# Kernel optimization log

Hardware: AMD Instinct MI355X
Metric: run time of the kernel (lower is better)

Reference implementation:

```python
import jax, jax.numpy as jnp
import numpy as np

NUM_NODES = 100000
HIDDEN = 128
HEADS = 4
NUM_EDGES = 1600000
NUM_PAIRS = 100000


def _leaky_relu(x, slope=0.2):
    return jnp.where(x >= 0, x, slope * x)


def _gat_layer(x, W, a_src, a_dst, src, dst):
    # x: [N, D]; W: [D, H*Dh]; a_src/a_dst: [H, Dh]
    N = x.shape[0]
    H, Dh = a_src.shape
    h = (x @ W).reshape(N, H, Dh)
    hs = h[src]                                   # [E, H, Dh] gather
    e = _leaky_relu((hs * a_src).sum(-1) + (h[dst] * a_dst).sum(-1))  # [E, H]
    # torch scatter_reduce amax over a zeros buffer => max clamped at 0
    m = jnp.maximum(jax.ops.segment_max(e, dst, num_segments=N), 0.0)  # [N, H]
    a = jnp.exp(e - m[dst])
    s = jax.ops.segment_sum(a, dst, num_segments=N)
    a = a / (s[dst] + 1e-10)
    out = jax.ops.segment_sum(hs * a[..., None], dst, num_segments=N)  # [N, H, Dh]
    return out.reshape(N, H * Dh)


def setup_inputs() -> dict:
    key = jax.random.key(0)
    ks = jax.random.split(key, 16)
    N, D, H = NUM_NODES, HIDDEN, HEADS
    Dh = D // H
    sW = float(np.sqrt(6.0 / (D + D)))
    sa = float(np.sqrt(6.0 / (H + Dh)))
    inp = {
        'embed': jax.random.uniform(ks[0], (N, D), jnp.float32, -sW, sW),
        'W1': jax.random.uniform(ks[1], (D, D), jnp.float32, -sW, sW),
        'a_src1': jax.random.uniform(ks[2], (H, Dh), jnp.float32, -sa, sa),
        'a_dst1': jax.random.uniform(ks[3], (H, Dh), jnp.float32, -sa, sa),
        'W2': jax.random.uniform(ks[4], (D, D), jnp.float32, -sW, sW),
        'a_src2': jax.random.uniform(ks[5], (H, Dh), jnp.float32, -sa, sa),
        'a_dst2': jax.random.uniform(ks[6], (H, Dh), jnp.float32, -sa, sa),
        'lp_w1': jax.random.uniform(ks[7], (2 * D, D), jnp.float32, -sW, sW),
        'lp_b1': jnp.zeros((D,), jnp.float32),
        'lp_w2': jax.random.uniform(ks[8], (D, 1), jnp.float32, -sW, sW),
        'lp_b2': jnp.zeros((1,), jnp.float32),
        'edge_index': jax.random.randint(ks[9], (2, NUM_EDGES), 0, N, jnp.int64 if jax.config.jax_enable_x64 else jnp.int32),
        'link_src': jax.random.randint(ks[10], (NUM_PAIRS,), 0, N),
        'link_dst': jax.random.randint(ks[11], (NUM_PAIRS,), 0, N),
    }
    return inp


def reference(embed, W1, a_src1, a_dst1, W2, a_src2, a_dst2,
              lp_w1, lp_b1, lp_w2, lp_b2, edge_index, link_src, link_dst):
    src, dst = edge_index[0], edge_index[1]
    x = embed
    x = jax.nn.elu(_gat_layer(x, W1, a_src1, a_dst1, src, dst)) + x
    x = jax.nn.elu(_gat_layer(x, W2, a_src2, a_dst2, src, dst)) + x
    z = x
    hcat = jnp.concatenate([z[link_src], z[link_dst]], axis=-1)  # [P, 2D]
    hid = jax.nn.relu(hcat @ lp_w1 + lp_b1)
    logits = (hid @ lp_w2 + lp_b2).squeeze(-1)  # [P]
    return logits
```

## Files before the change

### kernel.cpp

```cpp
#include <hip/hip_runtime.h>

typedef unsigned short u16;
typedef unsigned int u32;
typedef __attribute__((ext_vector_type(8))) short short8;
typedef __attribute__((ext_vector_type(4))) float float4v;

#define N_NODES 100000
#define N_EDGES 1600000
#define N_PAIRS 100000
#define NBUCKP 256
#define NB_USED 196
#define BUCK_CAP 8704
#define BIN_GRID 391

__device__ __forceinline__ float bf2f(u32 lo16) {
    union { u32 u; float f; } v;
    v.u = lo16 << 16;
    return v.f;
}
__device__ __forceinline__ u16 f2bf(float f) {
    union { float f; u32 u; } v;
    v.f = f;
    u32 r = v.u + 0x7fffu + ((v.u >> 16) & 1u);
    return (u16)(r >> 16);
}

#define FMIX_LO(A, Q, W) asm("v_fma_mix_f32 %0, %1, %2, %0 op_sel:[0,0,0] op_sel_hi:[1,1,0]" : "+v"(A) : "v"(Q), "v"(W))
#define FMIX_HI(A, Q, W) asm("v_fma_mix_f32 %0, %1, %2, %0 op_sel:[1,0,0] op_sel_hi:[1,1,0]" : "+v"(A) : "v"(Q), "v"(W))

__global__ __launch_bounds__(256) void k_prepB4(const float* __restrict__ W1, const float* __restrict__ W2,
                                                const float* __restrict__ WA, const float* __restrict__ WB,
                                                u16* __restrict__ B1, u16* __restrict__ B2,
                                                u16* __restrict__ BA, u16* __restrict__ BB,
                                                int* __restrict__ bucket_cur) {
    if (blockIdx.x == 32) {
        bucket_cur[threadIdx.x] = threadIdx.x * BUCK_CAP;
        return;
    }
    int w = blockIdx.x >> 3;
    const float* W = (w == 0) ? W1 : (w == 1) ? W2 : (w == 2) ? WA : WB;
    u16* Bf = (w == 0) ? B1 : (w == 1) ? B2 : (w == 2) ? BA : BB;
    int t = (blockIdx.x & 7) * 256 + threadIdx.x;
    int kk = t >> 9, tn = (t >> 6) & 7, quad = (t >> 4) & 3, l15 = t & 15;
#pragma unroll
    for (int j = 0; j < 8; j++) {
        int k = kk * 32 + quad * 8 + j;
        int n = tn * 16 + l15;
        Bf[(size_t)t * 8 + j] = f2bf(W[k * 128 + n]);
    }
}

__global__ __launch_bounds__(256) void k_bin(const int* __restrict__ esrc, const int* __restrict__ edst,
                                             int* bucket_cur, int2* __restrict__ binned) {
    __shared__ int cnt[NBUCKP];
    __shared__ int base[NBUCKP];
    int t = threadIdx.x;
    cnt[t] = 0;
    __syncthreads();
    int s[16], d[16], r[16];
    int e0 = blockIdx.x * 4096;
#pragma unroll
    for (int k = 0; k < 16; k++) {
        int e = e0 + k * 256 + t;
        if (e < N_EDGES) {
            s[k] = esrc[e];
            d[k] = edst[e];
            r[k] = atomicAdd(&cnt[d[k] >> 9], 1);
        } else {
            d[k] = -1;
        }
    }
    __syncthreads();
    base[t] = cnt[t] ? atomicAdd(&bucket_cur[t], cnt[t]) : 0;
    __syncthreads();
#pragma unroll
    for (int k = 0; k < 16; k++) {
        if (d[k] >= 0) {
            int bk = d[k] >> 9;
            int pos = base[bk] + r[k];
            if (pos < (bk + 1) * BUCK_CAP)
                binned[pos] = make_int2(s[k], d[k]);
        }
    }
}

__global__ __launch_bounds__(512) void k_sort(const int2* __restrict__ binned,
                                              const int* __restrict__ bucket_cur,
                                              int* __restrict__ row_ptr,
                                              int* __restrict__ col_src) {
    __shared__ int cnt[512];
    __shared__ int sm[512];
    int b = blockIdx.x, t = threadIdx.x;

    int partial = 0;
    if (t < b) partial = bucket_cur[t] - t * BUCK_CAP;
    sm[t] = partial;
    __syncthreads();
    for (int o = 256; o >= 1; o >>= 1) {
        if (t < o) sm[t] += sm[t + o];
        __syncthreads();
    }
    int base = sm[0];
    int n_e = bucket_cur[b] - b * BUCK_CAP;
    if (n_e > BUCK_CAP) n_e = BUCK_CAP;
    __syncthreads();

    cnt[t] = 0;
    __syncthreads();
    const int2* ebase = binned + (size_t)b * BUCK_CAP;
    for (int i = t; i < n_e; i += 512)
        atomicAdd(&cnt[ebase[i].y & 511], 1);
    __syncthreads();
    int v = cnt[t];
    sm[t] = v;
    __syncthreads();
    for (int o = 1; o < 512; o <<= 1) {
        int x = (t >= o) ? sm[t - o] : 0;
        __syncthreads();
        sm[t] += x;
        __syncthreads();
    }
    int excl = base + sm[t] - v;
    int node = b * 512 + t;
    if (node <= N_NODES) row_ptr[node] = excl;
    cnt[t] = excl;
    __syncthreads();
    for (int i = t; i < n_e; i += 512) {
        int2 sd = ebase[i];
        int p = atomicAdd(&cnt[sd.y & 511], 1);
        col_src[p] = sd.x;
    }
}

template<bool AF32, bool DUAL, bool QUANT>
__global__ __launch_bounds__(256) void k_gemm(const void* __restrict__ Ap,
                                              const u16* __restrict__ Bf,
                                              const u16* __restrict__ Bf2,
                                              u16* __restrict__ C,
                                              u16* __restrict__ C2,
                                              char* __restrict__ hq,
                                              float* __restrict__ alsc,
                                              const float* __restrict__ a_src,
                                              const float* __restrict__ a_dst,
                                              float* __restrict__ al_d, int M) {
    int wave = threadIdx.x >> 6, lane = threadIdx.x & 63;
    int quad = lane >> 4, l15 = lane & 15;
    int row0 = blockIdx.x * 64 + wave * 16;
    int m = row0 + l15;
    int mload = (m < M) ? m : (M - 1);

    short8 a[4];
    if (AF32) {
        const float* A = (const float*)Ap;
#pragma unroll
        for (int kk = 0; kk < 4; kk++) {
            const float* p = A + (size_t)mload * 128 + kk * 32 + quad * 8;
            float4 f0 = *(const float4*)p;
            float4 f1 = *(const float4*)(p + 4);
            short8 av;
            av[0] = (short)f2bf(f0.x); av[1] = (short)f2bf(f0.y);
            av[2] = (short)f2bf(f0.z); av[3] = (short)f2bf(f0.w);
            av[4] = (short)f2bf(f1.x); av[5] = (short)f2bf(f1.y);
            av[6] = (short)f2bf(f1.z); av[7] = (short)f2bf(f1.w);
            a[kk] = av;
        }
    } else {
        const u16* A = (const u16*)Ap;
#pragma unroll
        for (int kk = 0; kk < 4; kk++)
            a[kk] = *(const short8*)(A + (size_t)mload * 128 + kk * 32 + quad * 8);
    }

    float4v acc[8], acc2[8];
#pragma unroll
    for (int tn = 0; tn < 8; tn++) {
        acc[tn] = (float4v){0.f, 0.f, 0.f, 0.f};
        if (DUAL) acc2[tn] = (float4v){0.f, 0.f, 0.f, 0.f};
    }

#pragma unroll
    for (int kk = 0; kk < 4; kk++) {
#pragma unroll
        for (int tn = 0; tn < 8; tn++) {
            short8 b = *(const short8*)(Bf + ((size_t)((kk * 8 + tn) * 64 + lane)) * 8);
            acc[tn] = __builtin_amdgcn_mfma_f32_16x16x32_bf16(a[kk], b, acc[tn], 0, 0, 0);
            if (DUAL) {
                short8 b2 = *(const short8*)(Bf2 + ((size_t)((kk * 8 + tn) * 64 + lane)) * 8);
                acc2[tn] = __builtin_amdgcn_mfma_f32_16x16x32_bf16(a[kk], b2, acc2[tn], 0, 0, 0);
            }
        }
    }

    float as0[4], as1[4], ad0[4], ad1[4];
    if (QUANT) {
#pragma unroll
        for (int hd = 0; hd < 4; hd++) {
            as0[hd] = a_src[hd * 32 + l15];
            as1[hd] = a_src[hd * 32 + 16 + l15];
            ad0[hd] = a_dst[hd * 32 + l15];
            ad1[hd] = a_dst[hd * 32 + 16 + l15];
        }
    }

#pragma unroll
    for (int rg = 0; rg < 4; rg++) {
        int gr = row0 + quad * 4 + rg;
        bool ok = (gr < M);
        if (!QUANT) {
            if (ok) {
#pragma unroll
                for (int tn = 0; tn < 8; tn++) {
                    C[(size_t)gr * 128 + tn * 16 + l15] = f2bf(acc[tn][rg]);
                    if (DUAL) C2[(size_t)gr * 128 + tn * 16 + l15] = f2bf(acc2[tn][rg]);
                }
            }
        } else {
            float amax = 0.f;
#pragma unroll
            for (int tn = 0; tn < 8; tn++) amax = fmaxf(amax, fabsf(acc[tn][rg]));
#pragma unroll
            for (int mm = 1; mm < 16; mm <<= 1) amax = fmaxf(amax, __shfl_xor(amax, mm, 64));
            float inv_s = (amax > 0.f) ? 127.f / amax : 0.f;
            if (ok) {
#pragma unroll
                for (int tn = 0; tn < 8; tn++) {
                    int q = (int)rintf(acc[tn][rg] * inv_s);
                    hq[(size_t)gr * 128 + tn * 16 + l15] = (char)(q + 128);
                }
            }
            float ps[4], pd[4];
#pragma unroll
            for (int hd = 0; hd < 4; hd++) {
                float c0 = acc[2 * hd][rg];
                float c1 = acc[2 * hd + 1][rg];
                ps[hd] = c0 * as0[hd] + c1 * as1[hd];
                pd[hd] = c0 * ad0[hd] + c1 * ad1[hd];
            }
#pragma unroll
            for (int mm = 1; mm < 16; mm <<= 1) {
#pragma unroll
                for (int hd = 0; hd < 4; hd++) {
                    ps[hd] += __shfl_xor(ps[hd], mm, 64);
                    pd[hd] += __shfl_xor(pd[hd], mm, 64);
                }
            }
            if (ok && l15 < 4) {
                float vs = (l15 == 0) ? ps[0] : (l15 == 1) ? ps[1] : (l15 == 2) ? ps[2] : ps[3];
                float vd = (l15 == 0) ? pd[0] : (l15 == 1) ? pd[1] : (l15 == 2) ? pd[2] : pd[3];
                alsc[(size_t)gr * 8 + l15 * 2]     = vs;
                alsc[(size_t)gr * 8 + l15 * 2 + 1] = amax * (1.f / 127.f);
                al_d[gr * 4 + l15] = vd;
            }
        }
    }
}

template<bool XF32>
__global__ __launch_bounds__(256) void k_agg(const int* __restrict__ row_ptr, const int* __restrict__ col_src,
                      const float* __restrict__ alsc, const float* __restrict__ al_d,
                      const char* __restrict__ hq,
                      const void* __restrict__ xin, u16* __restrict__ xout) {
    int node = blockIdx.x * 4 + (threadIdx.x >> 6);
    int lane = threadIdx.x & 63;
    int l15 = lane & 15;
    int grp = lane >> 4;
    int bh  = l15 >> 2;
    int ae  = lane >> 2;
    int ah  = lane & 3;
    int beg = row_ptr[node], end = row_ptr[node + 1];
    int deg = end - beg;
    int degm1 = (deg > 0) ? deg - 1 : 0;
    float adst = al_d[node * 4 + ah];
    u32 loff = (u32)(l15 * 8);

    float sw = 0.f, swl = 0.f;
    u32 h_one = 0x3C00u;
    float acc[8];
#pragma unroll
    for (int k = 0; k < 8; k++) acc[k] = 0.f;

    int nch = (deg + 15) >> 4;
    for (int cb = 0; cb < nch; cb++) {
        int c = cb * 16;
        int idx = c + l15;
        idx = (idx <= degm1) ? idx : degm1;
        int sv = col_src[beg + idx];

        int sA = __shfl(sv, ae, 64);
        float2 av = *(const float2*)(alsc + ((size_t)sA << 3) + (ah << 1));
        float ev = av.x + adst;
        ev = fmaxf(ev, 0.2f * ev);
        float w = __expf(ev);
        w = ((c + ae) < deg) ? w : 0.f;
        sw += w;
        float wsc = w * av.y;

#pragma unroll
        for (int i = 0; i < 4; i++) {
            int slot = 4 * i + grp;
            int s = __shfl(sv, slot, 64);
            float wl = __shfl(wsc, slot * 4 + bh, 64);
            u32 wlh;
            asm("v_cvt_f16_f32 %0, %1" : "=v"(wlh) : "v"(wl));
            FMIX_LO(swl, h_one, wlh);
            u32 off = ((u32)s << 7) + loff;
            uint2 hv = *(const uint2*)(hq + off);
            u32 p01 = __builtin_amdgcn_perm(0x64646464u, hv.x, 0x04010400u);
            u32 p23 = __builtin_amdgcn_perm(0x64646464u, hv.x, 0x04030402u);
            u32 p45 = __builtin_amdgcn_perm(0x64646464u, hv.y, 0x04010400u);
            u32 p67 = __builtin_amdgcn_perm(0x64646464u, hv.y, 0x04030402u);
            FMIX_LO(acc[0], p01, wlh); FMIX_HI(acc[1], p01, wlh);
            FMIX_LO(acc[2], p23, wlh); FMIX_HI(acc[3], p23, wlh);
            FMIX_LO(acc[4], p45, wlh); FMIX_HI(acc[5], p45, wlh);
            FMIX_LO(acc[6], p67, wlh); FMIX_HI(acc[7], p67, wlh);
        }
    }

#pragma unroll
    for (int k = 0; k < 8; k++) acc[k] = fmaf(swl, -1152.f, acc[k]);

#pragma unroll
    for (int mm = 4; mm < 64; mm <<= 1) sw += __shfl_xor(sw, mm, 64);
    float inv = 1.f / (__shfl(sw, bh, 64) + 1e-10f);

#pragma unroll
    for (int k = 0; k < 8; k++) {
        acc[k] += __shfl_xor(acc[k], 16, 64);
        acc[k] += __shfl_xor(acc[k], 32, 64);
    }

    if (grp == 0) {
        float r[8];
        if (XF32) {
            const float* x = (const float*)xin;
            float4 x0 = *(const float4*)&x[(size_t)node * 128 + l15 * 8];
            float4 x1 = *(const float4*)&x[(size_t)node * 128 + l15 * 8 + 4];
            r[0] = x0.x; r[1] = x0.y; r[2] = x0.z; r[3] = x0.w;
            r[4] = x1.x; r[5] = x1.y; r[6] = x1.z; r[7] = x1.w;
        } else {
            const u16* x = (const u16*)xin;
            short8 xv = *(const short8*)&x[(size_t)node * 128 + l15 * 8];
#pragma unroll
            for (int k = 0; k < 8; k++) r[k] = bf2f((u16)xv[k]);
        }
        u32 ow[4];
#pragma unroll
        for (int k = 0; k < 4; k++) {
            float a0 = acc[2 * k] * inv;
            float a1 = acc[2 * k + 1] * inv;
            a0 = (a0 > 0.f) ? a0 : (__expf(a0) - 1.f);
            a1 = (a1 > 0.f) ? a1 : (__expf(a1) - 1.f);
            ow[k] = (u32)f2bf(a0 + r[2 * k]) | ((u32)f2bf(a1 + r[2 * k + 1]) << 16);
        }
        *(uint4*)&xout[(size_t)node * 128 + l15 * 8] = make_uint4(ow[0], ow[1], ow[2], ow[3]);
    }
}

__global__ void k_pair(const int* __restrict__ psrc, const int* __restrict__ pdst,
                       const u16* __restrict__ u, const u16* __restrict__ v,
                       const float* __restrict__ b1, const float* __restrict__ w2,
                       const float* __restrict__ b2, float* __restrict__ out) {
    int p = blockIdx.x * 4 + (threadIdx.x >> 6);
    int lane = threadIdx.x & 63;
    int s = psrc[p], d = pdst[p];
    float h0 = bf2f(u[(size_t)s * 128 + lane * 2])     + bf2f(v[(size_t)d * 128 + lane * 2])     + b1[lane * 2];
    float h1 = bf2f(u[(size_t)s * 128 + lane * 2 + 1]) + bf2f(v[(size_t)d * 128 + lane * 2 + 1]) + b1[lane * 2 + 1];
    h0 = (h0 > 0.f) ? h0 : 0.f;
    h1 = (h1 > 0.f) ? h1 : 0.f;
    float acc = h0 * w2[lane * 2] + h1 * w2[lane * 2 + 1];
#pragma unroll
    for (int m = 1; m < 64; m <<= 1) acc += __shfl_xor(acc, m, 64);
    if (lane == 0) out[p] = acc + b2[0];
}

extern "C" void kernel_launch(void* const* d_in, const int* in_sizes, int n_in,
                              void* d_out, int out_size, void* d_ws, size_t ws_size,
                              hipStream_t stream) {
    const float* embed  = (const float*)d_in[0];
    const float* W1     = (const float*)d_in[1];
    const float* a_src1 = (const float*)d_in[2];
    const float* a_dst1 = (const float*)d_in[3];
    const float* W2     = (const float*)d_in[4];
    const float* a_src2 = (const float*)d_in[5];
    const float* a_dst2 = (const float*)d_in[6];
    const float* lp_w1  = (const float*)d_in[7];
    const float* lp_b1  = (const float*)d_in[8];
    const float* lp_w2  = (const float*)d_in[9];
    const float* lp_b2  = (const float*)d_in[10];
    const int*   edge   = (const int*)d_in[11];
    const int*   lsrc   = (const int*)d_in[12];
    const int*   ldst   = (const int*)d_in[13];
    float* out = (float*)d_out;

    char* ws = (char*)d_ws;
    size_t off = 0;
    auto alloc = [&](size_t bytes) -> char* {
        char* p = ws + off;
        off += (bytes + 255) & ~(size_t)255;
        return p;
    };
    int*  row_ptr    = (int*)alloc((N_NODES + 1) * 4);
    int*  bucket_cur = (int*)alloc(NBUCKP * 4);
    int2* binned     = (int2*)alloc((size_t)NBUCKP * BUCK_CAP * 8);
    int*  col_src    = (int*)alloc((size_t)N_EDGES * 4);
    char* hq         = (char*)alloc((size_t)N_NODES * 128);
    float* alsc      = (float*)alloc((size_t)N_NODES * 8 * 4);
    float* al_d      = (float*)alloc((size_t)N_NODES * 4 * 4);
    u16*  x1         = (u16*)alloc((size_t)N_NODES * 128 * 2);
    u16*  z          = (u16*)alloc((size_t)N_NODES * 128 * 2);
    u16*  uu         = (u16*)alloc((size_t)N_NODES * 128 * 2);
    u16*  vv         = (u16*)alloc((size_t)N_NODES * 128 * 2);
    u16*  Bf1        = (u16*)alloc(128 * 128 * 2);
    u16*  Bf2        = (u16*)alloc(128 * 128 * 2);
    u16*  BfA        = (u16*)alloc(128 * 128 * 2);
    u16*  BfB        = (u16*)alloc(128 * 128 * 2);

    const int* esrc = edge;
    const int* edst = edge + N_EDGES;
    const int GB = (N_NODES + 63) / 64;

    k_prepB4<<<33, 256, 0, stream>>>(W1, W2, lp_w1, lp_w1 + 128 * 128, Bf1, Bf2, BfA, BfB, bucket_cur);

    k_bin <<<BIN_GRID, 256, 0, stream>>>(esrc, edst, bucket_cur, binned);
    k_sort<<<NB_USED, 512, 0, stream>>>(binned, bucket_cur, row_ptr, col_src);

    k_gemm<true, false, true><<<GB, 256, 0, stream>>>(embed, Bf1, nullptr, nullptr, nullptr,
                                                      hq, alsc, a_src1, a_dst1, al_d, N_NODES);
    k_agg<true><<<N_NODES / 4, 256, 0, stream>>>(row_ptr, col_src, alsc, al_d, hq, embed, x1);
    k_gemm<false, false, true><<<GB, 256, 0, stream>>>(x1, Bf2, nullptr, nullptr, nullptr,
                                                       hq, alsc, a_src2, a_dst2, al_d, N_NODES);
    k_agg<false><<<N_NODES / 4, 256, 0, stream>>>(row_ptr, col_src, alsc, al_d, hq, x1, z);
    k_gemm<false, true, false><<<GB, 256, 0, stream>>>(z, BfA, BfB, uu, vv,
                                                       nullptr, nullptr, nullptr, nullptr, nullptr, N_NODES);
    k_pair<<<N_PAIRS / 4, 256, 0, stream>>>(lsrc, ldst, uu, vv, lp_b1, lp_w2, lp_b2, out);
}
```

Baseline: 356.2 us.

## Unroll GAT aggregation for first 32 edges with all gathers issued upfront

Replaces the chunked 16-edge loop in the aggregation kernel with a fixed 32-edge prologue. All col_src, attention-score and feature-row gathers are issued before any use, which raises memory-level parallelism for typical degree-16 nodes. Edges past 32 go through a scalar per-edge tail loop, and zero-degree nodes exit early after writing the residual. The residual input load is hoisted to the start so its latency overlaps with the gathers. In exchange, nodes with fewer than 32 edges now do redundant clamped loads, and register pressure rises from the 8 outstanding feature loads.

```diff
diff --git a/kernel.cpp b/kernel.cpp
--- a/kernel.cpp
+++ b/kernel.cpp
@@ -269,46 +269,112 @@
     int ah  = lane & 3;
     int beg = row_ptr[node], end = row_ptr[node + 1];
     int deg = end - beg;
-    int degm1 = (deg > 0) ? deg - 1 : 0;
+    u32 loff = (u32)(l15 * 8);
+
+    float r[8];
+    if (XF32) {
+        const float* x = (const float*)xin;
+        float4 x0 = *(const float4*)&x[(size_t)node * 128 + l15 * 8];
+        float4 x1 = *(const float4*)&x[(size_t)node * 128 + l15 * 8 + 4];
+        r[0] = x0.x; r[1] = x0.y; r[2] = x0.z; r[3] = x0.w;
+        r[4] = x1.x; r[5] = x1.y; r[6] = x1.z; r[7] = x1.w;
+    } else {
+        const u16* x = (const u16*)xin;
+        short8 xv = *(const short8*)&x[(size_t)node * 128 + l15 * 8];
+#pragma unroll
+        for (int k = 0; k < 8; k++) r[k] = bf2f((u16)xv[k]);
+    }
+
+    if (deg == 0) {
+        if (grp == 0) {
+            u32 ow[4];
+#pragma unroll
+            for (int k = 0; k < 4; k++)
+                ow[k] = (u32)f2bf(r[2 * k]) | ((u32)f2bf(r[2 * k + 1]) << 16);
+            *(uint4*)&xout[(size_t)node * 128 + l15 * 8] = make_uint4(ow[0], ow[1], ow[2], ow[3]);
+        }
+        return;
+    }
+    int degm1 = deg - 1;
     float adst = al_d[node * 4 + ah];
-    u32 loff = (u32)(l15 * 8);
-
-    float sw = 0.f, swl = 0.f;
+
+    int slotA0 = (ae <= degm1) ? ae : degm1;
+    int slotA1 = (ae + 16 <= degm1) ? ae + 16 : degm1;
+    int sA0 = col_src[beg + slotA0];
+    int sA1 = col_src[beg + slotA1];
+    int sB[8];
+#pragma unroll
+    for (int i = 0; i < 8; i++) {
+        int slot = i * 4 + grp;
+        slot = (slot <= degm1) ? slot : degm1;
+        sB[i] = col_src[beg + slot];
+    }
+
+    float2 avA0 = *(const float2*)(alsc + ((size_t)sA0 << 3) + (ah << 1));
+    float2 avA1 = *(const float2*)(alsc + ((size_t)sA1 << 3) + (ah << 1));
+    uint2 hv[8];
+#pragma unroll
+    for (int i = 0; i < 8; i++)
+        hv[i] = *(const uint2*)(hq + (((u32)sB[i]) << 7) + loff);
+
+    float ev0 = avA0.x + adst;
+    ev0 = fmaxf(ev0, 0.2f * ev0);
+    float w0 = __expf(ev0);
+    w0 = (ae < deg) ? w0 : 0.f;
+    float ev1 = avA1.x + adst;
+    ev1 = fmaxf(ev1, 0.2f * ev1);
+    float w1 = __expf(ev1);
+    w1 = (ae + 16 < deg) ? w1 : 0.f;
+    float sw = w0 + w1;
+    float wsc0 = w0 * avA0.y;
+    float wsc1 = w1 * avA1.y;
+
+#pragma unroll
+    for (int mm = 4; mm < 64; mm <<= 1) sw += __shfl_xor(sw, mm, 64);
+
+    float swl = 0.f;
     u32 h_one = 0x3C00u;
     float acc[8];
 #pragma unroll
     for (int k = 0; k < 8; k++) acc[k] = 0.f;
 
-    int nch = (deg + 15) >> 4;
-    for (int cb = 0; cb < nch; cb++) {
-        int c = cb * 16;
-        int idx = c + l15;
-        idx = (idx <= degm1) ? idx : degm1;
-        int sv = col_src[beg + idx];
-
-        int sA = __shfl(sv, ae, 64);
-        float2 av = *(const float2*)(alsc + ((size_t)sA << 3) + (ah << 1));
-        float ev = av.x + adst;
-        ev = fmaxf(ev, 0.2f * ev);
-        float w = __expf(ev);
-        w = ((c + ae) < deg) ? w : 0.f;
-        sw += w;
-        float wsc = w * av.y;
-
-#pragma unroll
-        for (int i = 0; i < 4; i++) {
-            int slot = 4 * i + grp;
-            int s = __shfl(sv, slot, 64);
-            float wl = __shfl(wsc, slot * 4 + bh, 64);
+#pragma unroll
+    for (int i = 0; i < 8; i++) {
+        int slot = i * 4 + grp;
+        float wl = (i < 4) ? __shfl(wsc0, slot * 4 + bh, 64)
+                           : __shfl(wsc1, (slot - 16) * 4 + bh, 64);
+        u32 wlh;
+        asm("v_cvt_f16_f32 %0, %1" : "=v"(wlh) : "v"(wl));
+        FMIX_LO(swl, h_one, wlh);
+        u32 p01 = __builtin_amdgcn_perm(0x64646464u, hv[i].x, 0x04010400u);
+        u32 p23 = __builtin_amdgcn_perm(0x64646464u, hv[i].x, 0x04030402u);
+        u32 p45 = __builtin_amdgcn_perm(0x64646464u, hv[i].y, 0x04010400u);
+        u32 p67 = __builtin_amdgcn_perm(0x64646464u, hv[i].y, 0x04030402u);
+        FMIX_LO(acc[0], p01, wlh); FMIX_HI(acc[1], p01, wlh);
+        FMIX_LO(acc[2], p23, wlh); FMIX_HI(acc[3], p23, wlh);
+        FMIX_LO(acc[4], p45, wlh); FMIX_HI(acc[5], p45, wlh);
+        FMIX_LO(acc[6], p67, wlh); FMIX_HI(acc[7], p67, wlh);
+    }
+
+    float swt = 0.f;
+    if (deg > 32) {
+        float adstB = al_d[node * 4 + bh];
+        for (int i = 32; i < deg; i++) {
+            int s = __builtin_amdgcn_readfirstlane(col_src[beg + i]);
+            float2 av = *(const float2*)(alsc + ((size_t)s << 3) + (bh << 1));
+            float ev = av.x + adstB;
+            ev = fmaxf(ev, 0.2f * ev);
+            float w = __expf(ev);
+            swt += w;
+            float wl = (grp == 0) ? w * av.y : 0.f;
             u32 wlh;
             asm("v_cvt_f16_f32 %0, %1" : "=v"(wlh) : "v"(wl));
             FMIX_LO(swl, h_one, wlh);
-            u32 off = ((u32)s << 7) + loff;
-            uint2 hv = *(const uint2*)(hq + off);
-            u32 p01 = __builtin_amdgcn_perm(0x64646464u, hv.x, 0x04010400u);
-            u32 p23 = __builtin_amdgcn_perm(0x64646464u, hv.x, 0x04030402u);
-            u32 p45 = __builtin_amdgcn_perm(0x64646464u, hv.y, 0x04010400u);
-            u32 p67 = __builtin_amdgcn_perm(0x64646464u, hv.y, 0x04030402u);
+            uint2 hvt = *(const uint2*)(hq + (((u32)s) << 7) + loff);
+            u32 p01 = __builtin_amdgcn_perm(0x64646464u, hvt.x, 0x04010400u);
+            u32 p23 = __builtin_amdgcn_perm(0x64646464u, hvt.x, 0x04030402u);
+            u32 p45 = __builtin_amdgcn_perm(0x64646464u, hvt.y, 0x04010400u);
+            u32 p67 = __builtin_amdgcn_perm(0x64646464u, hvt.y, 0x04030402u);
             FMIX_LO(acc[0], p01, wlh); FMIX_HI(acc[1], p01, wlh);
             FMIX_LO(acc[2], p23, wlh); FMIX_HI(acc[3], p23, wlh);
             FMIX_LO(acc[4], p45, wlh); FMIX_HI(acc[5], p45, wlh);
@@ -319,9 +385,7 @@
 #pragma unroll
     for (int k = 0; k < 8; k++) acc[k] = fmaf(swl, -1152.f, acc[k]);
 
-#pragma unroll
-    for (int mm = 4; mm < 64; mm <<= 1) sw += __shfl_xor(sw, mm, 64);
-    float inv = 1.f / (__shfl(sw, bh, 64) + 1e-10f);
+    float inv = 1.f / (__shfl(sw, bh, 64) + swt + 1e-10f);
 
 #pragma unroll
     for (int k = 0; k < 8; k++) {
@@ -330,19 +394,6 @@
     }
 
     if (grp == 0) {
-        float r[8];
-        if (XF32) {
-            const float* x = (const float*)xin;
-            float4 x0 = *(const float4*)&x[(size_t)node * 128 + l15 * 8];
-            float4 x1 = *(const float4*)&x[(size_t)node * 128 + l15 * 8 + 4];
-            r[0] = x0.x; r[1] = x0.y; r[2] = x0.z; r[3] = x0.w;
-            r[4] = x1.x; r[5] = x1.y; r[6] = x1.z; r[7] = x1.w;
-        } else {
-            const u16* x = (const u16*)xin;
-            short8 xv = *(const short8*)&x[(size_t)node * 128 + l15 * 8];
-#pragma unroll
-            for (int k = 0; k < 8; k++) r[k] = bf2f((u16)xv[k]);
-        }
         u32 ow[4];
 #pragma unroll
         for (int k = 0; k < 4; k++) {
```

Result: no change. 358.5 us (+0.7%).

## Fuse link-predictor GEMM with pair gather into a single MFMA kernel

Applied to the files above, without the earlier changes.

Removes the dual GEMM that projected every node through both halves of lp_w1, and the separate pair kernel. A new kernel gathers z rows for each link pair directly as MFMA A operands, accumulates both halves into one accumulator, then applies bias, ReLU, the w2 dot product and a reduction in registers. This avoids writing and re-reading two N x 128 bf16 intermediates and one launch. The cost is a gathered, less coalesced A-operand load per pair. Rounding also changes slightly because the sum is kept in fp32 instead of being rounded to bf16 per half.

```diff
diff --git a/kernel.cpp b/kernel.cpp
--- a/kernel.cpp
+++ b/kernel.cpp
@@ -132,12 +132,10 @@
     }
 }
 
-template<bool AF32, bool DUAL, bool QUANT>
+template<bool AF32, bool QUANT>
 __global__ __launch_bounds__(256) void k_gemm(const void* __restrict__ Ap,
                                               const u16* __restrict__ Bf,
-                                              const u16* __restrict__ Bf2,
                                               u16* __restrict__ C,
-                                              u16* __restrict__ C2,
                                               char* __restrict__ hq,
                                               float* __restrict__ alsc,
                                               const float* __restrict__ a_src,
@@ -171,12 +169,9 @@
             a[kk] = *(const short8*)(A + (size_t)mload * 128 + kk * 32 + quad * 8);
     }
 
-    float4v acc[8], acc2[8];
-#pragma unroll
-    for (int tn = 0; tn < 8; tn++) {
-        acc[tn] = (float4v){0.f, 0.f, 0.f, 0.f};
-        if (DUAL) acc2[tn] = (float4v){0.f, 0.f, 0.f, 0.f};
-    }
+    float4v acc[8];
+#pragma unroll
+    for (int tn = 0; tn < 8; tn++) acc[tn] = (float4v){0.f, 0.f, 0.f, 0.f};
 
 #pragma unroll
     for (int kk = 0; kk < 4; kk++) {
@@ -184,10 +179,6 @@
         for (int tn = 0; tn < 8; tn++) {
             short8 b = *(const short8*)(Bf + ((size_t)((kk * 8 + tn) * 64 + lane)) * 8);
             acc[tn] = __builtin_amdgcn_mfma_f32_16x16x32_bf16(a[kk], b, acc[tn], 0, 0, 0);
-            if (DUAL) {
-                short8 b2 = *(const short8*)(Bf2 + ((size_t)((kk * 8 + tn) * 64 + lane)) * 8);
-                acc2[tn] = __builtin_amdgcn_mfma_f32_16x16x32_bf16(a[kk], b2, acc2[tn], 0, 0, 0);
-            }
         }
     }
 
@@ -209,10 +200,8 @@
         if (!QUANT) {
             if (ok) {
 #pragma unroll
-                for (int tn = 0; tn < 8; tn++) {
+                for (int tn = 0; tn < 8; tn++)
                     C[(size_t)gr * 128 + tn * 16 + l15] = f2bf(acc[tn][rg]);
-                    if (DUAL) C2[(size_t)gr * 128 + tn * 16 + l15] = f2bf(acc2[tn][rg]);
-                }
             }
         } else {
             float amax = 0.f;
@@ -356,21 +345,62 @@
     }
 }
 
-__global__ void k_pair(const int* __restrict__ psrc, const int* __restrict__ pdst,
-                       const u16* __restrict__ u, const u16* __restrict__ v,
-                       const float* __restrict__ b1, const float* __restrict__ w2,
-                       const float* __restrict__ b2, float* __restrict__ out) {
-    int p = blockIdx.x * 4 + (threadIdx.x >> 6);
-    int lane = threadIdx.x & 63;
-    int s = psrc[p], d = pdst[p];
-    float h0 = bf2f(u[(size_t)s * 128 + lane * 2])     + bf2f(v[(size_t)d * 128 + lane * 2])     + b1[lane * 2];
-    float h1 = bf2f(u[(size_t)s * 128 + lane * 2 + 1]) + bf2f(v[(size_t)d * 128 + lane * 2 + 1]) + b1[lane * 2 + 1];
-    h0 = (h0 > 0.f) ? h0 : 0.f;
-    h1 = (h1 > 0.f) ? h1 : 0.f;
-    float acc = h0 * w2[lane * 2] + h1 * w2[lane * 2 + 1];
-#pragma unroll
-    for (int m = 1; m < 64; m <<= 1) acc += __shfl_xor(acc, m, 64);
-    if (lane == 0) out[p] = acc + b2[0];
+__global__ __launch_bounds__(256) void k_link(const int* __restrict__ psrc, const int* __restrict__ pdst,
+                                              const u16* __restrict__ z,
+                                              const u16* __restrict__ BfA, const u16* __restrict__ BfB,
+                                              const float* __restrict__ b1, const float* __restrict__ w2,
+                                              const float* __restrict__ b2, float* __restrict__ out) {
+    int wave = threadIdx.x >> 6, lane = threadIdx.x & 63;
+    int quad = lane >> 4, l15 = lane & 15;
+    int row0 = blockIdx.x * 64 + wave * 16;
+    int prow = row0 + l15;
+    int pload = (prow < N_PAIRS) ? prow : (N_PAIRS - 1);
+    int s = psrc[pload], d = pdst[pload];
+
+    short8 a1[4], a2[4];
+#pragma unroll
+    for (int kk = 0; kk < 4; kk++) {
+        a1[kk] = *(const short8*)(z + (size_t)s * 128 + kk * 32 + quad * 8);
+        a2[kk] = *(const short8*)(z + (size_t)d * 128 + kk * 32 + quad * 8);
+    }
+
+    float4v acc[8];
+#pragma unroll
+    for (int tn = 0; tn < 8; tn++) acc[tn] = (float4v){0.f, 0.f, 0.f, 0.f};
+
+#pragma unroll
+    for (int kk = 0; kk < 4; kk++) {
+#pragma unroll
+        for (int tn = 0; tn < 8; tn++) {
+            short8 ba = *(const short8*)(BfA + ((size_t)((kk * 8 + tn) * 64 + lane)) * 8);
+            acc[tn] = __builtin_amdgcn_mfma_f32_16x16x32_bf16(a1[kk], ba, acc[tn], 0, 0, 0);
+            short8 bb = *(const short8*)(BfB + ((size_t)((kk * 8 + tn) * 64 + lane)) * 8);
+            acc[tn] = __builtin_amdgcn_mfma_f32_16x16x32_bf16(a2[kk], bb, acc[tn], 0, 0, 0);
+        }
+    }
+
+    float b1v[8], w2v[8];
+#pragma unroll
+    for (int tn = 0; tn < 8; tn++) {
+        b1v[tn] = b1[tn * 16 + l15];
+        w2v[tn] = w2[tn * 16 + l15];
+    }
+    float bb2 = b2[0];
+
+#pragma unroll
+    for (int rg = 0; rg < 4; rg++) {
+        float part = 0.f;
+#pragma unroll
+        for (int tn = 0; tn < 8; tn++) {
+            float h = acc[tn][rg] + b1v[tn];
+            h = (h > 0.f) ? h : 0.f;
+            part += h * w2v[tn];
+        }
+#pragma unroll
+        for (int mm = 1; mm < 16; mm <<= 1) part += __shfl_xor(part, mm, 64);
+        int gr = row0 + quad * 4 + rg;
+        if (l15 == 0 && gr < N_PAIRS) out[gr] = part + bb2;
+    }
 }
 
 extern "C" void kernel_launch(void* const* d_in, const int* in_sizes, int n_in,
@@ -408,8 +438,6 @@
     float* al_d      = (float*)alloc((size_t)N_NODES * 4 * 4);
     u16*  x1         = (u16*)alloc((size_t)N_NODES * 128 * 2);
     u16*  z          = (u16*)alloc((size_t)N_NODES * 128 * 2);
-    u16*  uu         = (u16*)alloc((size_t)N_NODES * 128 * 2);
-    u16*  vv         = (u16*)alloc((size_t)N_NODES * 128 * 2);
     u16*  Bf1        = (u16*)alloc(128 * 128 * 2);
     u16*  Bf2        = (u16*)alloc(128 * 128 * 2);
     u16*  BfA        = (u16*)alloc(128 * 128 * 2);
@@ -418,19 +446,18 @@
     const int* esrc = edge;
     const int* edst = edge + N_EDGES;
     const int GB = (N_NODES + 63) / 64;
+    const int GP = (N_PAIRS + 63) / 64;
 
     k_prepB4<<<33, 256, 0, stream>>>(W1, W2, lp_w1, lp_w1 + 128 * 128, Bf1, Bf2, BfA, BfB, bucket_cur);
 
     k_bin <<<BIN_GRID, 256, 0, stream>>>(esrc, edst, bucket_cur, binned);
     k_sort<<<NB_USED, 512, 0, stream>>>(binned, bucket_cur, row_ptr, col_src);
 
-    k_gemm<true, false, true><<<GB, 256, 0, stream>>>(embed, Bf1, nullptr, nullptr, nullptr,
-                                                      hq, alsc, a_src1, a_dst1, al_d, N_NODES);
+    k_gemm<true, true><<<GB, 256, 0, stream>>>(embed, Bf1, nullptr,
+                                               hq, alsc, a_src1, a_dst1, al_d, N_NODES);
     k_agg<true><<<N_NODES / 4, 256, 0, stream>>>(row_ptr, col_src, alsc, al_d, hq, embed, x1);
-    k_gemm<false, false, true><<<GB, 256, 0, stream>>>(x1, Bf2, nullptr, nullptr, nullptr,
-                                                       hq, alsc, a_src2, a_dst2, al_d, N_NODES);
+    k_gemm<false, true><<<GB, 256, 0, stream>>>(x1, Bf2, nullptr,
+                                                hq, alsc, a_src2, a_dst2, al_d, N_NODES);
     k_agg<false><<<N_NODES / 4, 256, 0, stream>>>(row_ptr, col_src, alsc, al_d, hq, x1, z);
-    k_gemm<false, true, false><<<GB, 256, 0, stream>>>(z, BfA, BfB, uu, vv,
-                                                       nullptr, nullptr, nullptr, nullptr, nullptr, N_NODES);
-    k_pair<<<N_PAIRS / 4, 256, 0, stream>>>(lsrc, ldst, uu, vv, lp_b1, lp_w2, lp_b2, out);
-}
+    k_link<<<GP, 256, 0, stream>>>(lsrc, ldst, z, BfA, BfB, lp_b1, lp_w2, lp_b2, out);
+}
```

After: 328.7 us. 7.7% less time.
